# Performance work log

Measured on AMD Instinct MI355X. Metric: run time of the kernel, lower is better.

The kernel has to match this reference:

```python
import jax, jax.numpy as jnp
import numpy as np

N = 100000
E = 1600000
C_IN = 128
C_OUT = 128
EPS = 1e-5


def setup_inputs() -> dict:
    key = jax.random.key(0)
    ks = jax.random.split(key, 8)
    x = jax.random.normal(ks[0], (N, C_IN), dtype=jnp.float32)
    edge_index = jax.random.randint(ks[1], (2, E), 0, N, dtype=jnp.int64)
    s_proj = 1.0 / np.sqrt(C_IN)
    s_out = 1.0 / np.sqrt(C_IN)
    W_proj = jax.random.uniform(ks[2], (C_IN, C_IN), jnp.float32, -s_proj, s_proj)
    b_proj = jax.random.uniform(ks[3], (C_IN,), jnp.float32, -s_proj, s_proj)
    W_l = jax.random.uniform(ks[4], (C_OUT, C_IN), jnp.float32, -s_out, s_out)
    b_l = jax.random.uniform(ks[5], (C_OUT,), jnp.float32, -s_out, s_out)
    W_r = jax.random.uniform(ks[6], (C_OUT, C_IN), jnp.float32, -s_out, s_out)
    gamma = jnp.ones((C_OUT,), jnp.float32)
    beta = jnp.zeros((C_OUT,), jnp.float32)
    return {"x": x, "edge_index": edge_index, "W_proj": W_proj, "b_proj": b_proj,
            "W_l": W_l, "b_l": b_l, "W_r": W_r, "gamma": gamma, "beta": beta}


def reference(x, edge_index, W_proj, b_proj, W_l, b_l, W_r, gamma, beta):
    # SAGEConv(project=True, aggr='sum'): project+ReLU source features per node,
    # gather along edges, scatter-sum at targets, then lin_l(agg) + lin_r(x_root).
    src, dst = edge_index[0], edge_index[1]
    h = jax.nn.relu(x @ W_proj.T + b_proj)            # [N, C_IN]
    msg = h[src]                                       # [E, C_IN] edge gather
    agg = jax.ops.segment_sum(msg, dst, num_segments=N)  # [N, C_IN]
    out = agg @ W_l.T + b_l + x @ W_r.T                # [N, C_OUT] (root uses unprojected x)
    # LayerNorm(c_out)
    mu = jnp.mean(out, axis=-1, keepdims=True)
    var = jnp.var(out, axis=-1, keepdims=True)
    return (out - mu) * jax.lax.rsqrt(var + EPS) * gamma + beta
```

## Files before the change

kernel.cpp:

```cpp
#include <hip/hip_runtime.h>
#include <stdint.h>

#define NN 100000
#define NE 1600000
#define C  128
#define NB 782
#define CAP 4096
#define SB_SHIFT 13
#define GEMMB 1564
#define P1B 250
#define MBO 782

typedef __attribute__((ext_vector_type(8))) short short8;
typedef __attribute__((ext_vector_type(4))) float f32x4;

__device__ __forceinline__ float bf2f(uint16_t u) {
  union { uint32_t u; float f; } v; v.u = ((uint32_t)u) << 16; return v.f;
}
__device__ __forceinline__ uint16_t f2bf(float f) {
  union { float f; uint32_t u; } v; v.f = f;
  uint32_t r = v.u + 0x7fffu + ((v.u >> 16) & 1u);
  return (uint16_t)(r >> 16);
}
__device__ __forceinline__ float2 bf2x2(uint32_t u) {
  return make_float2(bf2f((uint16_t)u), bf2f((uint16_t)(u >> 16)));
}

__global__ __launch_bounds__(256) void cast3_k(
    const float* __restrict__ a, const float* __restrict__ b, const float* __restrict__ c,
    uint16_t* __restrict__ oa, uint16_t* __restrict__ ob, uint16_t* __restrict__ oc)
{
  int i = blockIdx.x * 256 + threadIdx.x;
  int which = i >> 12, j = i & 4095;
  const float* s = which == 0 ? a : (which == 1 ? b : c);
  uint16_t* d    = which == 0 ? oa : (which == 1 ? ob : oc);
  float4 v = ((const float4*)s)[j];
  uint2 p;
  p.x = (uint32_t)f2bf(v.x) | ((uint32_t)f2bf(v.y) << 16);
  p.y = (uint32_t)f2bf(v.z) | ((uint32_t)f2bf(v.w) << 16);
  ((uint2*)d)[j] = p;
}


__global__ __launch_bounds__(512) void fused_front_k(
    const float* __restrict__ x, const uint16_t* __restrict__ wpb,
    const uint16_t* __restrict__ wrb,
    const float* __restrict__ bp, const float* __restrict__ bl,
    uint16_t* __restrict__ h, uint16_t* __restrict__ rb,
    const int* __restrict__ esrc, const int* __restrict__ edst,
    int* __restrict__ gcnt, uint32_t* __restrict__ ebuf)
{
  extern __shared__ uint8_t slds[];
  const int t = threadIdx.x;

  if (blockIdx.x < GEMMB) {
    const int half  = blockIdx.x & 1;
    const int rtile = blockIdx.x >> 1;
#pragma unroll
    for (int qq = 0; qq < 4; ++qq) {
      int ci = qq * 512 + t;
      int m  = ci >> 10;
      int cj = ci & 1023;
      int cl = cj >> 4, k16 = cj & 15;
      const uint16_t* wsrc = m == 0 ? wpb : wrb;
      *(short8*)(slds + m * 16384 + cl * 256 + ((k16 ^ (cl & 15)) << 4)) =
          *(const short8*)(wsrc + ((size_t)(half * 64 + cl) * 16 + k16) * 8);
    }
    __syncthreads();

    const int w = t >> 6, lane = t & 63;
    const int tile_m = rtile * 128 + w * 16;
    if (tile_m >= NN) return;
    const int r16 = lane & 15, g = lane >> 4;

    const int row = tile_m + r16;
    const int arow = row < NN ? row : NN - 1;
    short8 a[4];
    const float* xp = x + (size_t)arow * C + g * 8;
#pragma unroll
    for (int kk = 0; kk < 4; ++kk) {
      float4 u = *(const float4*)(xp + kk * 32);
      float4 v = *(const float4*)(xp + kk * 32 + 4);
      short8 av;
      av[0] = (short)f2bf(u.x); av[1] = (short)f2bf(u.y);
      av[2] = (short)f2bf(u.z); av[3] = (short)f2bf(u.w);
      av[4] = (short)f2bf(v.x); av[5] = (short)f2bf(v.y);
      av[6] = (short)f2bf(v.z); av[7] = (short)f2bf(v.w);
      a[kk] = av;
    }

#pragma unroll
    for (int nt = 0; nt < 4; ++nt) {
      f32x4 hp = {0.f, 0.f, 0.f, 0.f};
      f32x4 hr = {0.f, 0.f, 0.f, 0.f};
      const int cl = nt * 16 + r16;
      const uint8_t* rbp = slds + cl * 256;
      const uint8_t* rbr = slds + 16384 + cl * 256;
#pragma unroll
      for (int kk = 0; kk < 4; ++kk) {
        int slot = (((kk << 2) + g) ^ (cl & 15)) << 4;
        hp = __builtin_amdgcn_mfma_f32_16x16x32_bf16(*(const short8*)(rbp + slot), a[kk], hp, 0, 0, 0);
        hr = __builtin_amdgcn_mfma_f32_16x16x32_bf16(*(const short8*)(rbr + slot), a[kk], hr, 0, 0, 0);
      }
      const int col0 = half * 64 + nt * 16 + g * 4;
      float4 bp4 = *(const float4*)(bp + col0);
      float4 bl4 = *(const float4*)(bl + col0);
      if (row < NN) {
        float h0 = hp[0] + bp4.x, h1 = hp[1] + bp4.y, h2 = hp[2] + bp4.z, h3 = hp[3] + bp4.w;
        h0 = h0 > 0.f ? h0 : 0.f; h1 = h1 > 0.f ? h1 : 0.f;
        h2 = h2 > 0.f ? h2 : 0.f; h3 = h3 > 0.f ? h3 : 0.f;
        uint2 ph;
        ph.x = (uint32_t)f2bf(h0) | ((uint32_t)f2bf(h1) << 16);
        ph.y = (uint32_t)f2bf(h2) | ((uint32_t)f2bf(h3) << 16);
        *(uint2*)(h + (size_t)row * C + col0) = ph;
        uint2 pr;
        pr.x = (uint32_t)f2bf(hr[0] + bl4.x) | ((uint32_t)f2bf(hr[1] + bl4.y) << 16);
        pr.y = (uint32_t)f2bf(hr[2] + bl4.z) | ((uint32_t)f2bf(hr[3] + bl4.w) << 16);
        *(uint2*)(rb + (size_t)row * C + col0) = pr;
      }
    }
  } else {
    int* bh = (int*)slds;
    int* gb = bh + NB;
    const int blk = blockIdx.x - GEMMB;
    const int base = blk * 6400;

    for (int i = t; i < NB; i += 512) bh[i] = 0;

    const int4* ed4 = (const int4*)(edst + base);
    const int4* es4 = (const int4*)(esrc + base);
    int4 dv[4], sv[4];
    bool val[4];
#pragma unroll
    for (int k = 0; k < 4; ++k) {
      int i = t + k * 512;
      val[k] = (i < 1600);
      if (val[k]) { dv[k] = ed4[i]; sv[k] = es4[i]; }
    }
    __syncthreads();

#pragma unroll
    for (int k = 0; k < 4; ++k) if (val[k]) {
      atomicAdd(&bh[dv[k].x >> 7], 1); atomicAdd(&bh[dv[k].y >> 7], 1);
      atomicAdd(&bh[dv[k].z >> 7], 1); atomicAdd(&bh[dv[k].w >> 7], 1);
    }
    __syncthreads();

    for (int i = t; i < NB; i += 512) {
      int c = bh[i];
      gb[i] = c ? atomicAdd(&gcnt[i], c) : 0;
      bh[i] = 0;
    }
    __syncthreads();

#define P1_SCATTER(d, s) do { \
      int bb = (d) >> 7; \
      int o = atomicAdd(&bh[bb], 1); \
      int pos = gb[bb] + o; \
      if (pos < CAP) ebuf[(size_t)bb * CAP + pos] = ((uint32_t)((d) & 127) << 17) | (uint32_t)(s); \
    } while (0)

#pragma unroll
    for (int k = 0; k < 4; ++k) if (val[k]) {
      P1_SCATTER(dv[k].x, sv[k].x); P1_SCATTER(dv[k].y, sv[k].y);
      P1_SCATTER(dv[k].z, sv[k].z); P1_SCATTER(dv[k].w, sv[k].w);
    }
#undef P1_SCATTER
  }
}

__global__ __launch_bounds__(256) void phase2_k(
    const uint32_t* __restrict__ ebuf, const int* __restrict__ gcnt,
    int* __restrict__ ssrc, int2* __restrict__ sdeg)
{
  __shared__ uint32_t raw[CAP];
  __shared__ int lout[CAP];
  __shared__ int cnt2[128 * 16];
  __shared__ int nd[128];
  __shared__ int psum[256];
  const int b = blockIdx.x, t = threadIdx.x;
  const int n0 = b * 128;

  int acc = 0;
  for (int i = t; i < b; i += 256) acc += gcnt[i];
  psum[t] = acc;
  __syncthreads();
  for (int off = 128; off > 0; off >>= 1) {
    if (t < off) psum[t] += psum[t + off];
    __syncthreads();
  }
  const int base = psum[0];
  int cnt = gcnt[b]; if (cnt > CAP) cnt = CAP;

  for (int i = t; i < 128 * 16; i += 256) cnt2[i] = 0;
  __syncthreads();
  for (int i = t; i < cnt; i += 256) {
    uint32_t v = ebuf[(size_t)b * CAP + i];
    raw[i] = v;
    atomicAdd(&cnt2[(v >> 17) * 16 + ((v & 0x1FFFFu) >> SB_SHIFT)], 1);
  }
  __syncthreads();

  int deg_t = 0;
  if (t < 128) {
#pragma unroll
    for (int i = 0; i < 16; ++i) deg_t += cnt2[t * 16 + i];
    nd[t] = deg_t;
  }
  __syncthreads();
  for (int off = 1; off < 128; off <<= 1) {
    int v = 0;
    if (t < 128 && t >= off) v = nd[t - off];
    __syncthreads();
    if (t < 128) nd[t] += v;
    __syncthreads();
  }
  if (t < 128) {
    int pref = nd[t] - deg_t;
    if (n0 + t < NN) sdeg[n0 + t] = make_int2(base + pref, deg_t);
    int run = pref;
#pragma unroll
    for (int i = 0; i < 16; ++i) { int c = cnt2[t * 16 + i]; cnt2[t * 16 + i] = run; run += c; }
  }
  __syncthreads();
  for (int i = t; i < cnt; i += 256) {
    uint32_t v = raw[i];
    int o = atomicAdd(&cnt2[(v >> 17) * 16 + ((v & 0x1FFFFu) >> SB_SHIFT)], 1);
    lout[o] = (int)(v & 0x1FFFFu);
  }
  __syncthreads();
  for (int i = t; i < cnt; i += 256) ssrc[base + i] = lout[i];
}

__global__ __launch_bounds__(256) void aggregate_k(
    const uint16_t* __restrict__ h, const int* __restrict__ ssrc,
    const int2* __restrict__ sdeg, uint16_t* __restrict__ agg)
{
  const int wid = (blockIdx.x * 256 + threadIdx.x) >> 6;
  if (wid >= NN) return;
  const int lane = threadIdx.x & 63;
  const int q = lane >> 4;
  const int l16 = lane & 15;
  const int2 sd = sdeg[wid];
  const int s0 = sd.x, cnt = sd.y;
  const size_t choff = (size_t)l16 * 8;
  float2 a0 = {0.f, 0.f}, a1 = {0.f, 0.f}, a2 = {0.f, 0.f}, a3 = {0.f, 0.f};

#define ACC8(v) do { \
    a0 += bf2x2((v).x); a1 += bf2x2((v).y); \
    a2 += bf2x2((v).z); a3 += bf2x2((v).w); \
  } while (0)

  if (cnt > 0) {
    int e0 = ssrc[s0 + ((q      < cnt) ? q      : cnt - 1)];
    int e1 = ssrc[s0 + ((q + 4  < cnt) ? q + 4  : cnt - 1)];
    int e2 = ssrc[s0 + ((q + 8  < cnt) ? q + 8  : cnt - 1)];
    int e3 = ssrc[s0 + ((q + 12 < cnt) ? q + 12 : cnt - 1)];
    for (int j = 0; j < cnt; j += 16) {
      uint4 v0 = *(const uint4*)(h + (size_t)e0 * C + choff);
      uint4 v1 = *(const uint4*)(h + (size_t)e1 * C + choff);
      uint4 v2 = *(const uint4*)(h + (size_t)e2 * C + choff);
      uint4 v3 = *(const uint4*)(h + (size_t)e3 * C + choff);
      const int jn = j + 16;
      if (jn < cnt) {
        e0 = ssrc[s0 + ((jn + q      < cnt) ? jn + q      : cnt - 1)];
        e1 = ssrc[s0 + ((jn + q + 4  < cnt) ? jn + q + 4  : cnt - 1)];
        e2 = ssrc[s0 + ((jn + q + 8  < cnt) ? jn + q + 8  : cnt - 1)];
        e3 = ssrc[s0 + ((jn + q + 12 < cnt) ? jn + q + 12 : cnt - 1)];
      }
      if (j + q      < cnt) ACC8(v0);
      if (j + q + 4  < cnt) ACC8(v1);
      if (j + q + 8  < cnt) ACC8(v2);
      if (j + q + 12 < cnt) ACC8(v3);
    }
  }
#undef ACC8

#pragma unroll
  for (int msk = 16; msk <= 32; msk <<= 1) {
    a0.x += __shfl_xor(a0.x, msk, 64); a0.y += __shfl_xor(a0.y, msk, 64);
    a1.x += __shfl_xor(a1.x, msk, 64); a1.y += __shfl_xor(a1.y, msk, 64);
    a2.x += __shfl_xor(a2.x, msk, 64); a2.y += __shfl_xor(a2.y, msk, 64);
    a3.x += __shfl_xor(a3.x, msk, 64); a3.y += __shfl_xor(a3.y, msk, 64);
  }
  if (q == 0) {
    uint4 p;
    p.x = (uint32_t)f2bf(a0.x) | ((uint32_t)f2bf(a0.y) << 16);
    p.y = (uint32_t)f2bf(a1.x) | ((uint32_t)f2bf(a1.y) << 16);
    p.z = (uint32_t)f2bf(a2.x) | ((uint32_t)f2bf(a2.y) << 16);
    p.w = (uint32_t)f2bf(a3.x) | ((uint32_t)f2bf(a3.y) << 16);
    *(uint4*)(agg + (size_t)wid * C + choff) = p;
  }
}

__global__ __launch_bounds__(512) void gemm_out_k(
    const uint16_t* __restrict__ aggb, const uint16_t* __restrict__ rb,
    const uint16_t* __restrict__ wlb, const float* __restrict__ gamma,
    const float* __restrict__ beta, float* __restrict__ out)
{
  __shared__ uint8_t wl[32768];
  const int t = threadIdx.x;
#pragma unroll
  for (int qq = 0; qq < 4; ++qq) {
    int ci = qq * 512 + t;
    int c = ci >> 4, k16 = ci & 15;
    *(short8*)(wl + c * 256 + ((k16 ^ (c & 15)) << 4)) = *(const short8*)(wlb + ci * 8);
  }
  __syncthreads();

  const int w = t >> 6, lane = t & 63;
  const int tile_m = blockIdx.x * 128 + w * 16;
  if (tile_m >= NN) return;
  const int r16 = lane & 15, g = lane >> 4;

  const int row = tile_m + r16;
  const int arow = row < NN ? row : NN - 1;
  short8 a0[4];
  const uint16_t* p0 = aggb + (size_t)arow * C + g * 8;
#pragma unroll
  for (int kk = 0; kk < 4; ++kk) a0[kk] = *(const short8*)(p0 + kk * 32);

  f32x4 acc[8];
  float s1 = 0.f, s2 = 0.f;
#pragma unroll
  for (int nt = 0; nt < 8; ++nt) {
    f32x4 c4 = {0.f, 0.f, 0.f, 0.f};
    const int c = nt * 16 + r16;
    const uint8_t* rbl = wl + c * 256;
#pragma unroll
    for (int kk = 0; kk < 4; ++kk) {
      short8 b = *(const short8*)(rbl + ((((kk << 2) + g) ^ (c & 15)) << 4));
      c4 = __builtin_amdgcn_mfma_f32_16x16x32_bf16(b, a0[kk], c4, 0, 0, 0);
    }
    const int col0 = nt * 16 + g * 4;
    uint2 rv = *(const uint2*)(rb + (size_t)arow * C + col0);
    float2 r01 = bf2x2(rv.x), r23 = bf2x2(rv.y);
    c4[0] += r01.x; c4[1] += r01.y; c4[2] += r23.x; c4[3] += r23.y;
#pragma unroll
    for (int rr = 0; rr < 4; ++rr) { s1 += c4[rr]; s2 += c4[rr] * c4[rr]; }
    acc[nt] = c4;
  }

  s1 += __shfl_xor(s1, 16, 64); s2 += __shfl_xor(s2, 16, 64);
  s1 += __shfl_xor(s1, 32, 64); s2 += __shfl_xor(s2, 32, 64);
  const float mean = s1 * (1.f / C);
  const float var = s2 * (1.f / C) - mean * mean;
  const float rstd = rsqrtf(var + 1e-5f);

  if (row < NN) {
#pragma unroll
    for (int nt = 0; nt < 8; ++nt) {
      const int col0 = nt * 16 + g * 4;
      float4 gm = *(const float4*)(gamma + col0);
      float4 bt = *(const float4*)(beta + col0);
      float4 o;
      o.x = (acc[nt][0] - mean) * rstd * gm.x + bt.x;
      o.y = (acc[nt][1] - mean) * rstd * gm.y + bt.y;
      o.z = (acc[nt][2] - mean) * rstd * gm.z + bt.z;
      o.w = (acc[nt][3] - mean) * rstd * gm.w + bt.w;
      *(float4*)(out + (size_t)row * C + col0) = o;
    }
  }
}

extern "C" void kernel_launch(void* const* d_in, const int* in_sizes, int n_in,
                              void* d_out, int out_size, void* d_ws, size_t ws_size,
                              hipStream_t stream)
{
  const float* x        = (const float*)d_in[0];
  const int* ei         = (const int*)d_in[1];
  const float* Wp       = (const float*)d_in[2];
  const float* bp       = (const float*)d_in[3];
  const float* Wl       = (const float*)d_in[4];
  const float* bl       = (const float*)d_in[5];
  const float* Wr       = (const float*)d_in[6];
  const float* gamma    = (const float*)d_in[7];
  const float* beta     = (const float*)d_in[8];
  float* out            = (float*)d_out;

  char* ws = (char*)d_ws;
  uint16_t* rb   = (uint16_t*)(ws + 0);
  uint16_t* h    = (uint16_t*)(ws + 25600000);
  uint32_t* ebuf = (uint32_t*)(ws + 51200000);
  uint16_t* aggb = (uint16_t*)(ws + 51200000);
  uint16_t* wpb  = (uint16_t*)(ws + 76800000);
  uint16_t* wlb  = (uint16_t*)(ws + 76832768);
  uint16_t* wrb  = (uint16_t*)(ws + 76865536);
  int2* sdeg     = (int2*)(ws + 76898304);
  int* gcnt      = (int*)(ws + 77698304);
  int* ssrc      = (int*)(ws + 78102400);

  const int* esrc = ei;
  const int* edst = ei + NE;

  hipMemsetAsync(gcnt, 0, NB * sizeof(int), stream);

  cast3_k<<<48, 256, 0, stream>>>(Wp, Wl, Wr, wpb, wlb, wrb);

  fused_front_k<<<GEMMB + P1B, 512, 32768, stream>>>(
      x, wpb, wrb, bp, bl, h, rb, esrc, edst, gcnt, ebuf);

  phase2_k<<<NB, 256, 0, stream>>>(ebuf, gcnt, ssrc, sdeg);

  aggregate_k<<<(NN + 3) / 4, 256, 0, stream>>>(h, ssrc, sdeg, aggb);

  gemm_out_k<<<MBO, 512, 0, stream>>>(aggb, rb, wlb, gamma, beta, out);
}
```

Measured before the change: 152.1 us.

## Compute full 128 output columns per block and stage stores through LDS

Each GEMM block in the fused front kernel now computes all 128 output columns for its 128 rows instead of half. This halves the block count and avoids loading and converting x twice. Results are written to a swizzled LDS tile and then stored to global memory as coalesced 16-byte rows. The trade-off is double the LDS (64KB), more accumulator registers per thread and extra barriers, which may reduce occupancy.

```diff
diff --git a/kernel.cpp b/kernel.cpp
--- a/kernel.cpp
+++ b/kernel.cpp
@@ -7,7 +7,7 @@
 #define NB 782
 #define CAP 4096
 #define SB_SHIFT 13
-#define GEMMB 1564
+#define MB 782
 #define P1B 250
 #define MBO 782
 
@@ -53,28 +53,25 @@
   extern __shared__ uint8_t slds[];
   const int t = threadIdx.x;
 
-  if (blockIdx.x < GEMMB) {
-    const int half  = blockIdx.x & 1;
-    const int rtile = blockIdx.x >> 1;
-#pragma unroll
-    for (int qq = 0; qq < 4; ++qq) {
+  if (blockIdx.x < MB) {
+#pragma unroll
+    for (int qq = 0; qq < 8; ++qq) {
       int ci = qq * 512 + t;
-      int m  = ci >> 10;
-      int cj = ci & 1023;
+      int m  = ci >> 11;
+      int cj = ci & 2047;
       int cl = cj >> 4, k16 = cj & 15;
       const uint16_t* wsrc = m == 0 ? wpb : wrb;
-      *(short8*)(slds + m * 16384 + cl * 256 + ((k16 ^ (cl & 15)) << 4)) =
-          *(const short8*)(wsrc + ((size_t)(half * 64 + cl) * 16 + k16) * 8);
+      *(short8*)(slds + m * 32768 + cl * 256 + ((k16 ^ (cl & 15)) << 4)) =
+          *(const short8*)(wsrc + cj * 8);
     }
     __syncthreads();
 
     const int w = t >> 6, lane = t & 63;
-    const int tile_m = rtile * 128 + w * 16;
-    if (tile_m >= NN) return;
+    const int tile_m0 = blockIdx.x * 128;
     const int r16 = lane & 15, g = lane >> 4;
-
-    const int row = tile_m + r16;
+    const int row = tile_m0 + w * 16 + r16;
     const int arow = row < NN ? row : NN - 1;
+
     short8 a[4];
     const float* xp = x + (size_t)arow * C + g * 8;
 #pragma unroll
@@ -89,40 +86,61 @@
       a[kk] = av;
     }
 
-#pragma unroll
-    for (int nt = 0; nt < 4; ++nt) {
-      f32x4 hp = {0.f, 0.f, 0.f, 0.f};
-      f32x4 hr = {0.f, 0.f, 0.f, 0.f};
-      const int cl = nt * 16 + r16;
-      const uint8_t* rbp = slds + cl * 256;
-      const uint8_t* rbr = slds + 16384 + cl * 256;
+    f32x4 hp[8], hr[8];
+#pragma unroll
+    for (int nt = 0; nt < 8; ++nt) {
+      f32x4 p = {0.f, 0.f, 0.f, 0.f};
+      f32x4 r = {0.f, 0.f, 0.f, 0.f};
+      const int cidx = nt * 16 + r16;
+      const uint8_t* rbp = slds + cidx * 256;
+      const uint8_t* rbr = slds + 32768 + cidx * 256;
 #pragma unroll
       for (int kk = 0; kk < 4; ++kk) {
-        int slot = (((kk << 2) + g) ^ (cl & 15)) << 4;
-        hp = __builtin_amdgcn_mfma_f32_16x16x32_bf16(*(const short8*)(rbp + slot), a[kk], hp, 0, 0, 0);
-        hr = __builtin_amdgcn_mfma_f32_16x16x32_bf16(*(const short8*)(rbr + slot), a[kk], hr, 0, 0, 0);
+        int slot = (((kk << 2) + g) ^ (cidx & 15)) << 4;
+        p = __builtin_amdgcn_mfma_f32_16x16x32_bf16(*(const short8*)(rbp + slot), a[kk], p, 0, 0, 0);
+        r = __builtin_amdgcn_mfma_f32_16x16x32_bf16(*(const short8*)(rbr + slot), a[kk], r, 0, 0, 0);
       }
-      const int col0 = half * 64 + nt * 16 + g * 4;
+      hp[nt] = p; hr[nt] = r;
+    }
+    __syncthreads();
+
+    const int lrow = w * 16 + r16;
+#pragma unroll
+    for (int nt = 0; nt < 8; ++nt) {
+      const int col0 = nt * 16 + g * 4;
       float4 bp4 = *(const float4*)(bp + col0);
       float4 bl4 = *(const float4*)(bl + col0);
-      if (row < NN) {
-        float h0 = hp[0] + bp4.x, h1 = hp[1] + bp4.y, h2 = hp[2] + bp4.z, h3 = hp[3] + bp4.w;
-        h0 = h0 > 0.f ? h0 : 0.f; h1 = h1 > 0.f ? h1 : 0.f;
-        h2 = h2 > 0.f ? h2 : 0.f; h3 = h3 > 0.f ? h3 : 0.f;
-        uint2 ph;
-        ph.x = (uint32_t)f2bf(h0) | ((uint32_t)f2bf(h1) << 16);
-        ph.y = (uint32_t)f2bf(h2) | ((uint32_t)f2bf(h3) << 16);
-        *(uint2*)(h + (size_t)row * C + col0) = ph;
-        uint2 pr;
-        pr.x = (uint32_t)f2bf(hr[0] + bl4.x) | ((uint32_t)f2bf(hr[1] + bl4.y) << 16);
-        pr.y = (uint32_t)f2bf(hr[2] + bl4.z) | ((uint32_t)f2bf(hr[3] + bl4.w) << 16);
-        *(uint2*)(rb + (size_t)row * C + col0) = pr;
+      float h0 = hp[nt][0] + bp4.x, h1 = hp[nt][1] + bp4.y;
+      float h2 = hp[nt][2] + bp4.z, h3 = hp[nt][3] + bp4.w;
+      h0 = h0 > 0.f ? h0 : 0.f; h1 = h1 > 0.f ? h1 : 0.f;
+      h2 = h2 > 0.f ? h2 : 0.f; h3 = h3 > 0.f ? h3 : 0.f;
+      uint2 ph, pr;
+      ph.x = (uint32_t)f2bf(h0) | ((uint32_t)f2bf(h1) << 16);
+      ph.y = (uint32_t)f2bf(h2) | ((uint32_t)f2bf(h3) << 16);
+      pr.x = (uint32_t)f2bf(hr[nt][0] + bl4.x) | ((uint32_t)f2bf(hr[nt][1] + bl4.y) << 16);
+      pr.y = (uint32_t)f2bf(hr[nt][2] + bl4.z) | ((uint32_t)f2bf(hr[nt][3] + bl4.w) << 16);
+      const int ioff = (col0 * 2) ^ ((lrow & 15) << 4);
+      *(uint2*)(slds + lrow * 256 + ioff) = ph;
+      *(uint2*)(slds + 32768 + lrow * 256 + ioff) = pr;
+    }
+    __syncthreads();
+
+#pragma unroll
+    for (int i = 0; i < 4; ++i) {
+      const int ofs = i * 8192 + t * 16;
+      const int trow = ofs >> 8;
+      const int inrow = ofs & 255;
+      const int grow = tile_m0 + trow;
+      const int phys = (trow << 8) + (inrow ^ ((trow & 15) << 4));
+      if (grow < NN) {
+        *(uint4*)(h  + (size_t)grow * C + (inrow >> 1)) = *(const uint4*)(slds + phys);
+        *(uint4*)(rb + (size_t)grow * C + (inrow >> 1)) = *(const uint4*)(slds + 32768 + phys);
       }
     }
   } else {
     int* bh = (int*)slds;
     int* gb = bh + NB;
-    const int blk = blockIdx.x - GEMMB;
+    const int blk = blockIdx.x - MB;
     const int base = blk * 6400;
 
     for (int i = t; i < NB; i += 512) bh[i] = 0;
@@ -397,7 +415,7 @@
 
   cast3_k<<<48, 256, 0, stream>>>(Wp, Wl, Wr, wpb, wlb, wrb);
 
-  fused_front_k<<<GEMMB + P1B, 512, 32768, stream>>>(
+  fused_front_k<<<MB + P1B, 512, 65536, stream>>>(
       x, wpb, wrb, bp, bl, h, rb, esrc, edst, gcnt, ebuf);
 
   phase2_k<<<NB, 256, 0, stream>>>(ebuf, gcnt, ssrc, sdeg);
```

New measurement: 141.0 us. -7.3%, faster.
